# Performance work log

Measured on AMD Instinct MI355X. Metric: run time of the kernel, lower is better.

The kernel has to match this reference:

```python
import jax, jax.numpy as jnp
import numpy as np

S = 1024          # num tokens (single prefill sequence)
H = 2880          # hidden_size
NH = 64           # num query heads
NKV = 8           # num kv heads
HD = 64           # head_dim
G = NH // NKV     # query heads per kv head
THETA = 10000.0
SCALE = HD ** -0.5


def _rope(x, positions):
    # neox-style rotary over full head_dim; x: [S, n_heads, HD]
    half = HD // 2
    inv_freq = 1.0 / (THETA ** (jnp.arange(half, dtype=jnp.float32) / half))
    ang = positions.astype(jnp.float32)[:, None] * inv_freq          # [S, half]
    cos = jnp.cos(ang)[:, None, :]
    sin = jnp.sin(ang)[:, None, :]
    x1, x2 = x[..., :half], x[..., half:]
    return jnp.concatenate([x1 * cos - x2 * sin, x2 * cos + x1 * sin], axis=-1)


def setup_inputs() -> dict:
    key = jax.random.key(0)
    k0, k1, k2, k3 = jax.random.split(key, 4)
    return {
        "positions": jnp.arange(S, dtype=jnp.int32),
        "hidden_states": jax.random.normal(k0, (S, H), dtype=jnp.float32),
        "qkv_w": jax.random.normal(k1, ((NH + 2 * NKV) * HD, H), dtype=jnp.float32) * 0.02,
        "o_w": jax.random.normal(k2, (H, NH * HD), dtype=jnp.float32) * 0.02,
        "sinks": jax.random.normal(k3, (NH,), dtype=jnp.float32),
    }


def reference(positions, hidden_states, qkv_w, o_w, sinks):
    # fused QKV projection (no bias, matching attention_bias=False)
    qkv = hidden_states @ qkv_w.T                                     # [S, 5120]
    q = qkv[:, : NH * HD].reshape(S, NH, HD)
    k = qkv[:, NH * HD : NH * HD + NKV * HD].reshape(S, NKV, HD)
    v = qkv[:, NH * HD + NKV * HD :].reshape(S, NKV, HD)

    # rotary on q and k (rotary_dim == head_dim)
    q = _rope(q, positions)
    k = _rope(k, positions)

    # GQA: group query heads by kv head -> [S, NKV, G, HD]
    qg = q.reshape(S, NKV, G, HD)

    logits = jnp.einsum("qghd,kgd->ghqk", qg, k) * SCALE              # [NKV, G, S, S]
    causal = positions[:, None] >= positions[None, :]                 # [S, S]
    logits = jnp.where(causal[None, None], logits, -jnp.inf)

    # attention sinks: per-head extra logit in the softmax denominator,
    # contributing no value vector.
    sink = sinks.reshape(NKV, G)[:, :, None, None]                    # [NKV, G, 1, 1]
    m = jnp.maximum(jnp.max(logits, axis=-1, keepdims=True), sink)
    p = jnp.exp(logits - m)                                           # [NKV, G, S, S]
    denom = jnp.sum(p, axis=-1, keepdims=True) + jnp.exp(sink - m)
    attn = jnp.einsum("ghqk,kgd->qghd", p / denom, v)                 # [S, NKV, G, HD]

    out = attn.reshape(S, NH * HD) @ o_w.T                            # [S, H]
    return out
```

## Files before the change

### kernel.cpp

```cpp
#include <hip/hip_runtime.h>
#include <hip/hip_bf16.h>
#include <math.h>

#define S_LEN 1024
#define HDIM  2880
#define NH    64
#define NKV   8
#define HD    64
#define QKV_N ((NH + 2*NKV) * HD)
#define O_K   (NH * HD)
#define SCALE 0.125f

typedef _Float16 f16x8 __attribute__((ext_vector_type(8)));
typedef _Float16 f16x4 __attribute__((ext_vector_type(4)));
typedef float    f32x4 __attribute__((ext_vector_type(4)));

#define DMA16(GP, LP) __builtin_amdgcn_global_load_lds( \
        (const __attribute__((address_space(1))) void*)(GP), \
        (__attribute__((address_space(3))) void*)(LP), 16, 0, 0)

#define BARRIER() __builtin_amdgcn_s_barrier()
#define WAITV(n)  asm volatile("s_waitcnt vmcnt(" #n ")" ::: "memory")
#define WAITL()   asm volatile("s_waitcnt lgkmcnt(0)" ::: "memory")
#define SCHED0()  __builtin_amdgcn_sched_barrier(0)

__device__ __forceinline__ void cvt4(const float* __restrict__ s,
                                     _Float16* __restrict__ d, int i) {
    const float4 v = ((const float4*)s)[i];
    f16x4 p;
    p[0] = (_Float16)v.x; p[1] = (_Float16)v.y;
    p[2] = (_Float16)v.z; p[3] = (_Float16)v.w;
    ((f16x4*)d)[i] = p;
}

__global__ __launch_bounds__(256) void cvt_f32_f16(const float* __restrict__ src,
                                                   _Float16* __restrict__ dst, int n4) {
    const int stride = gridDim.x * blockDim.x;
    for (int i = blockIdx.x * blockDim.x + threadIdx.x; i < n4; i += stride)
        cvt4(src, dst, i);
}

__global__ __launch_bounds__(256) void cvt_all(const float* __restrict__ h,
                                               const float* __restrict__ qw,
                                               const float* __restrict__ ow,
                                               _Float16* __restrict__ dh,
                                               _Float16* __restrict__ dqw,
                                               _Float16* __restrict__ dow) {
    const int stride = gridDim.x * blockDim.x;
    const int t0 = blockIdx.x * blockDim.x + threadIdx.x;
    for (int i = t0; i < 737280;  i += stride) cvt4(h,  dh,  i);
    for (int i = t0; i < 3686400; i += stride) cvt4(qw, dqw, i);
    for (int i = t0; i < 2949120; i += stride) cvt4(ow, dow, i);
}

__device__ __forceinline__ f16x8 lds_frag(const _Float16* base, int row, int kf) {
    return *(const f16x8*)&base[row * 64 + (kf ^ ((row & 7) << 3))];
}

__device__ __forceinline__ void mfma_quad(f32x4 (&acc)[8][4], const f16x8 (&af)[4][2],
                                          const f16x8 (&bf)[2][2], int mh, int nh) {
    __builtin_amdgcn_s_setprio(1);
#pragma unroll
    for (int q4 = 0; q4 < 4; ++q4)
#pragma unroll
        for (int n2 = 0; n2 < 2; ++n2) {
            f32x4 a = acc[mh * 4 + q4][nh * 2 + n2];
            a = __builtin_amdgcn_mfma_f32_16x16x32_f16(af[q4][0], bf[n2][0], a, 0, 0, 0);
            a = __builtin_amdgcn_mfma_f32_16x16x32_f16(af[q4][1], bf[n2][1], a, 0, 0, 0);
            acc[mh * 4 + q4][nh * 2 + n2] = a;
        }
    __builtin_amdgcn_s_setprio(0);
}

__global__ __launch_bounds__(512, 2) void gemm_8p(const _Float16* __restrict__ A,
                                                  const _Float16* __restrict__ B,
                                                  _Float16* __restrict__ C,
                                                  int M, int N, int K) {
    __shared__ __align__(16) _Float16 sh[65536];

    const int tid  = threadIdx.x;
    const int lane = tid & 63;
    const int wave = tid >> 6;
    const int wr   = wave >> 2;
    const int wc   = wave & 3;
    const int quad = lane >> 4;
    const int fr   = lane & 15;
    const int row0 = blockIdx.y * 256;
    const int col0 = blockIdx.x * 256;

    const int klen = K / (int)gridDim.z;
    const int kb   = (int)blockIdx.z * klen;
    const int NT   = klen / 64;
    _Float16* Cp = C + (size_t)blockIdx.z * M * N;

    int    stDst[2];
    size_t aOff[2][2], bOff[2][2];
#pragma unroll
    for (int r = 0; r < 2; ++r) {
        const int c   = r * 512 + tid;
        const int row = c >> 3;
        const int sw  = ((c & 7) ^ (row & 7)) * 8;
        stDst[r] = (c & ~63) * 8;
#pragma unroll
        for (int h = 0; h < 2; ++h) {
            aOff[h][r] = (size_t)(row0 + h * 128 + row) * K + sw;
            int br = col0 + h * 128 + row; if (br > N - 1) br = N - 1;
            bOff[h][r] = (size_t)br * K + sw;
        }
    }
    const _Float16* Ab = A + kb;
    const _Float16* Bb = B + kb;

#define STAGE2(GB, OFF, LB) do { \
        DMA16((GB) + (OFF)[0], (LB) + stDst[0]); \
        DMA16((GB) + (OFF)[1], (LB) + stDst[1]); } while (0)

    f32x4 acc[8][4] = {};

    STAGE2(Ab, aOff[0], sh);
    STAGE2(Ab, aOff[1], sh + 8192);
    STAGE2(Bb, bOff[0], sh + 32768);
    STAGE2(Bb, bOff[1], sh + 32768 + 8192);
    if (NT > 1) {
        STAGE2(Ab + 64, aOff[0], sh + 16384);
        STAGE2(Ab + 64, aOff[1], sh + 16384 + 8192);
        WAITV(4);
    } else {
        WAITV(0);
    }
    BARRIER();

    for (int t = 0; t < NT; ++t) {
        _Float16* Ac = sh + ((t & 1) ? 16384 : 0);
        _Float16* Bc = sh + 32768 + ((t & 1) ? 16384 : 0);
        _Float16* Bn = sh + 32768 + ((t & 1) ? 0 : 16384);
        const bool st1 = (t + 1 < NT);
        const bool st2 = (t + 2 < NT);
        const int  k1  = (t + 1) * 64;
        const int  k2  = (t + 2) * 64;

        f16x8 aF0[4][2], aF1[4][2], bF[2][2];

#pragma unroll
        for (int q4 = 0; q4 < 4; ++q4) {
            const int row = wr * 128 + q4 * 16 + fr;
            aF0[q4][0] = lds_frag(Ac, row, quad * 8);
            aF0[q4][1] = lds_frag(Ac, row, 32 + quad * 8);
        }
#pragma unroll
        for (int n2 = 0; n2 < 2; ++n2) {
            const int row = wc * 64 + n2 * 16 + fr;
            bF[n2][0] = lds_frag(Bc, row, quad * 8);
            bF[n2][1] = lds_frag(Bc, row, 32 + quad * 8);
        }
        if (st1) STAGE2(Bb + k1, bOff[0], Bn);
        BARRIER(); WAITL(); SCHED0();
        mfma_quad(acc, aF0, bF, 0, 0);
        BARRIER();

#pragma unroll
        for (int q4 = 0; q4 < 4; ++q4) {
            const int row = wr * 128 + 64 + q4 * 16 + fr;
            aF1[q4][0] = lds_frag(Ac, row, quad * 8);
            aF1[q4][1] = lds_frag(Ac, row, 32 + quad * 8);
        }
        if (st1) STAGE2(Bb + k1, bOff[1], Bn + 8192);
        BARRIER(); WAITL(); SCHED0();
        mfma_quad(acc, aF1, bF, 1, 0);
        BARRIER();

#pragma unroll
        for (int n2 = 0; n2 < 2; ++n2) {
            const int row = wc * 64 + 32 + n2 * 16 + fr;
            bF[n2][0] = lds_frag(Bc, row, quad * 8);
            bF[n2][1] = lds_frag(Bc, row, 32 + quad * 8);
        }
        if (st2) STAGE2(Ab + k2, aOff[0], Ac);
        BARRIER(); WAITL(); SCHED0();
        mfma_quad(acc, aF1, bF, 1, 1);
        BARRIER();

        if (st2) {
            STAGE2(Ab + k2, aOff[1], Ac + 8192);
            WAITV(4);
        } else {
            WAITV(0);
        }
        BARRIER(); WAITL(); SCHED0();
        mfma_quad(acc, aF0, bF, 0, 1);
        BARRIER();
    }

    __syncthreads();
    _Float16* cbuf = sh;
#pragma unroll
    for (int h = 0; h < 2; ++h) {
        if (wr == h) {
#pragma unroll
            for (int mi = 0; mi < 8; ++mi)
#pragma unroll
                for (int ni = 0; ni < 4; ++ni) {
                    const f32x4 v = acc[mi][ni];
#pragma unroll
                    for (int rr = 0; rr < 4; ++rr)
                        cbuf[(mi * 16 + quad * 4 + rr) * 264 + wc * 64 + ni * 16 + fr] =
                            (_Float16)v[rr];
                }
        }
        __syncthreads();
#pragma unroll
        for (int u = 0; u < 8; ++u) {
            const int c    = u * 512 + tid;
            const int rowL = c >> 5;
            const int ch   = (c & 31) * 8;
            const int col  = col0 + ch;
            if (col < N)
                *(f16x8*)&Cp[(size_t)(row0 + h * 128 + rowL) * N + col] =
                    *(const f16x8*)&cbuf[rowL * 264 + ch];
        }
        __syncthreads();
    }
#undef STAGE2
}

#define CSTR 68
template<typename CT>
__global__ __launch_bounds__(256) void gemm_ff(const _Float16* __restrict__ A,
                                               const _Float16* __restrict__ B,
                                               CT* __restrict__ C,
                                               int M, int N, int K) {
    __shared__ __align__(16) _Float16 sh[16384];

    const int tid  = threadIdx.x;
    const int lane = tid & 63;
    const int wave = tid >> 6;
    const int wr   = wave >> 1;
    const int wc   = wave & 1;
    const int quad = lane >> 4;
    const int fr   = lane & 15;
    const int ks   = quad * 8;
    const int row0 = blockIdx.y * 128;
    const int col0 = blockIdx.x * 128;

    const int klen   = K / (int)gridDim.z;
    const int kb     = (int)blockIdx.z * klen;
    const int nsteps = klen / 32;
    CT* Cp = C + (size_t)blockIdx.z * M * N;

    const int r0   = tid >> 2;
    const int ch   = (tid & 3) * 8;
    const int dst0 = (tid & ~63) * 8;

    const size_t aoff0 = (size_t)(row0 + r0)      * K;
    const size_t aoff1 = (size_t)(row0 + r0 + 64) * K;
    int bR0 = col0 + r0;      if (bR0 >= N) bR0 = N - 1;
    int bR1 = col0 + r0 + 64; if (bR1 >= N) bR1 = N - 1;
    const size_t boff0 = (size_t)bR0 * K;
    const size_t boff1 = (size_t)bR1 * K;

    f32x4 acc[4][4] = {};

    {
        const int kk = kb + ch;
        DMA16(A + aoff0 + kk, sh + dst0);
        DMA16(A + aoff1 + kk, sh + 2048 + dst0);
        DMA16(B + boff0 + kk, sh + 8192 + dst0);
        DMA16(B + boff1 + kk, sh + 8192 + 2048 + dst0);
    }

    for (int step = 0; step < nsteps; ++step) {
        const int cur = step & 1;
        _Float16* Acur = sh + cur * 4096;
        _Float16* Anxt = sh + (cur ^ 1) * 4096;
        _Float16* Bcur = sh + 8192 + cur * 4096;
        _Float16* Bnxt = sh + 8192 + (cur ^ 1) * 4096;

        __syncthreads();

        if (step + 1 < nsteps) {
            const int k1 = kb + (step + 1) * 32 + ch;
            DMA16(A + aoff0 + k1, Anxt + dst0);
            DMA16(A + aoff1 + k1, Anxt + 2048 + dst0);
            DMA16(B + boff0 + k1, Bnxt + dst0);
            DMA16(B + boff1 + k1, Bnxt + 2048 + dst0);
        }

        f16x8 af[4], bf[4];
#pragma unroll
        for (int mi = 0; mi < 4; ++mi)
            af[mi] = *(const f16x8*)&Acur[(wr * 64 + mi * 16 + fr) * 32 + ks];
#pragma unroll
        for (int ni = 0; ni < 4; ++ni)
            bf[ni] = *(const f16x8*)&Bcur[(wc * 64 + ni * 16 + fr) * 32 + ks];
#pragma unroll
        for (int mi = 0; mi < 4; ++mi)
#pragma unroll
            for (int ni = 0; ni < 4; ++ni)
                acc[mi][ni] = __builtin_amdgcn_mfma_f32_16x16x32_f16(
                    af[mi], bf[ni], acc[mi][ni], 0, 0, 0);
    }

#pragma unroll
    for (int p = 0; p < 2; ++p) {
        __syncthreads();
        if (wc == p) {
#pragma unroll
            for (int mi = 0; mi < 4; ++mi)
#pragma unroll
                for (int ni = 0; ni < 4; ++ni) {
                    const f32x4 v = acc[mi][ni];
#pragma unroll
                    for (int r = 0; r < 4; ++r)
                        sh[(wr * 64 + mi * 16 + quad * 4 + r) * CSTR + ni * 16 + fr] =
                            (_Float16)v[r];
                }
        }
        __syncthreads();
#pragma unroll
        for (int it = 0; it < 4; ++it) {
            const int id  = it * 256 + tid;
            const int row = id >> 3;
            const int chh = (id & 7) * 8;
            const int col = col0 + p * 64 + chh;
            if (col < N) {
                const f16x4 lo = *(const f16x4*)&sh[row * CSTR + chh];
                const f16x4 hi = *(const f16x4*)&sh[row * CSTR + chh + 4];
                if constexpr (sizeof(CT) == 2) {
                    f16x8 v;
                    v[0]=lo[0]; v[1]=lo[1]; v[2]=lo[2]; v[3]=lo[3];
                    v[4]=hi[0]; v[5]=hi[1]; v[6]=hi[2]; v[7]=hi[3];
                    *(f16x8*)&Cp[(size_t)(row0 + row) * N + col] = v;
                } else {
                    float4 v0 = make_float4((float)lo[0], (float)lo[1],
                                            (float)lo[2], (float)lo[3]);
                    float4 v1 = make_float4((float)hi[0], (float)hi[1],
                                            (float)hi[2], (float)hi[3]);
                    *(float4*)&Cp[(size_t)(row0 + row) * N + col]     = v0;
                    *(float4*)&Cp[(size_t)(row0 + row) * N + col + 4] = v1;
                }
            }
        }
    }
}

template<typename CT>
__global__ __launch_bounds__(256) void gemm_f16(const _Float16* __restrict__ A,
                                                const float* __restrict__ B,
                                                CT* __restrict__ C,
                                                int M, int N, int K) {
    __shared__ __align__(16) _Float16 sh[16384];

    const int tid  = threadIdx.x;
    const int lane = tid & 63;
    const int wave = tid >> 6;
    const int wr   = wave >> 1;
    const int wc   = wave & 1;
    const int quad = lane >> 4;
    const int fr   = lane & 15;
    const int ks   = quad * 8;
    const int row0 = blockIdx.y * 128;
    const int col0 = blockIdx.x * 128;

    const int klen   = K / (int)gridDim.z;
    const int kb     = (int)blockIdx.z * klen;
    const int nsteps = klen / 32;
    CT* Cp = C + (size_t)blockIdx.z * M * N;

    const int a_cbase0 = wave * 64;
    const int a_ci0 = a_cbase0 + lane;
    const int a_r0 = a_ci0 >> 2, a_ch0 = a_ci0 & 3;
    const int a_cbase1 = 256 + wave * 64;
    const int a_ci1 = a_cbase1 + lane;
    const int a_r1 = a_ci1 >> 2, a_ch1 = a_ci1 & 3;
    int b_r[4], b_ch[4];
#pragma unroll
    for (int it = 0; it < 4; ++it) {
        const int c4 = it * 256 + tid;
        b_r[it]  = c4 >> 3;
        b_ch[it] = (c4 & 7) << 2;
    }

    float4 breg[4];
    f32x4 acc[4][4] = {};

    {
        const _Float16* gp0 = A + (size_t)(row0 + a_r0) * K + kb + a_ch0 * 8;
        DMA16(gp0, sh + (size_t)a_cbase0 * 8);
        const _Float16* gp1 = A + (size_t)(row0 + a_r1) * K + kb + a_ch1 * 8;
        DMA16(gp1, sh + (size_t)a_cbase1 * 8);
#pragma unroll
        for (int it = 0; it < 4; ++it) {
            int brow = col0 + b_r[it];
            if (brow >= N) brow = N - 1;
            breg[it] = *(const float4*)&B[(size_t)brow * K + kb + b_ch[it]];
        }
        _Float16* Bs0 = sh + 8192;
#pragma unroll
        for (int it = 0; it < 4; ++it) {
            f16x4 p;
            p[0] = (_Float16)breg[it].x; p[1] = (_Float16)breg[it].y;
            p[2] = (_Float16)breg[it].z; p[3] = (_Float16)breg[it].w;
            *(f16x4*)&Bs0[b_r[it] * 32 + b_ch[it]] = p;
        }
    }

    for (int step = 0; step < nsteps; ++step) {
        const int cur = step & 1;
        const int nxt = cur ^ 1;
        _Float16* Acur = sh + cur * 4096;
        _Float16* Anxt = sh + nxt * 4096;
        _Float16* Bcur = sh + 8192 + cur * 4096;
        _Float16* Bnxt = sh + 8192 + nxt * 4096;

        __syncthreads();

        const bool more = (step + 1 < nsteps);
        if (more) {
            const int k1 = kb + (step + 1) * 32;
            const _Float16* gp0 = A + (size_t)(row0 + a_r0) * K + k1 + a_ch0 * 8;
            DMA16(gp0, Anxt + (size_t)a_cbase0 * 8);
            const _Float16* gp1 = A + (size_t)(row0 + a_r1) * K + k1 + a_ch1 * 8;
            DMA16(gp1, Anxt + (size_t)a_cbase1 * 8);
#pragma unroll
            for (int it = 0; it < 4; ++it) {
                int brow = col0 + b_r[it];
                if (brow >= N) brow = N - 1;
                breg[it] = *(const float4*)&B[(size_t)brow * K + k1 + b_ch[it]];
            }
        }

        f16x8 af[4], bfr[4];
#pragma unroll
        for (int mi = 0; mi < 4; ++mi)
            af[mi] = *(const f16x8*)&Acur[(wr * 64 + mi * 16 + fr) * 32 + ks];
#pragma unroll
        for (int ni = 0; ni < 4; ++ni)
            bfr[ni] = *(const f16x8*)&Bcur[(wc * 64 + ni * 16 + fr) * 32 + ks];
#pragma unroll
        for (int mi = 0; mi < 4; ++mi)
#pragma unroll
            for (int ni = 0; ni < 4; ++ni)
                acc[mi][ni] = __builtin_amdgcn_mfma_f32_16x16x32_f16(
                    af[mi], bfr[ni], acc[mi][ni], 0, 0, 0);

        if (more) {
#pragma unroll
            for (int it = 0; it < 4; ++it) {
                f16x4 p;
                p[0] = (_Float16)breg[it].x; p[1] = (_Float16)breg[it].y;
                p[2] = (_Float16)breg[it].z; p[3] = (_Float16)breg[it].w;
                *(f16x4*)&Bnxt[b_r[it] * 32 + b_ch[it]] = p;
            }
        }
    }

#pragma unroll
    for (int p = 0; p < 2; ++p) {
        __syncthreads();
        if (wc == p) {
#pragma unroll
            for (int mi = 0; mi < 4; ++mi)
#pragma unroll
                for (int ni = 0; ni < 4; ++ni) {
                    const f32x4 v = acc[mi][ni];
#pragma unroll
                    for (int r = 0; r < 4; ++r)
                        sh[(wr * 64 + mi * 16 + quad * 4 + r) * CSTR + ni * 16 + fr] =
                            (_Float16)v[r];
                }
        }
        __syncthreads();
#pragma unroll
        for (int it = 0; it < 4; ++it) {
            const int id  = it * 256 + tid;
            const int row = id >> 3;
            const int chh = (id & 7) * 8;
            const int col = col0 + p * 64 + chh;
            if (col < N) {
                const f16x4 lo = *(const f16x4*)&sh[row * CSTR + chh];
                const f16x4 hi = *(const f16x4*)&sh[row * CSTR + chh + 4];
                if constexpr (sizeof(CT) == 2) {
                    f16x8 v;
                    v[0]=lo[0]; v[1]=lo[1]; v[2]=lo[2]; v[3]=lo[3];
                    v[4]=hi[0]; v[5]=hi[1]; v[6]=hi[2]; v[7]=hi[3];
                    *(f16x8*)&Cp[(size_t)(row0 + row) * N + col] = v;
                } else {
                    float4 v0 = make_float4((float)lo[0], (float)lo[1],
                                            (float)lo[2], (float)lo[3]);
                    float4 v1 = make_float4((float)hi[0], (float)hi[1],
                                            (float)hi[2], (float)hi[3]);
                    *(float4*)&Cp[(size_t)(row0 + row) * N + col]     = v0;
                    *(float4*)&Cp[(size_t)(row0 + row) * N + col + 4] = v1;
                }
            }
        }
    }
}

__global__ __launch_bounds__(256) void rope_reduce(_Float16* __restrict__ parts,
                                                   int nsplit,
                                                   _Float16* __restrict__ vt,
                                                   const int* __restrict__ positions) {
    __shared__ float buf[QKV_N];
    const int s   = blockIdx.x;
    const int tid = threadIdx.x;
    const size_t PSTR = (size_t)S_LEN * QKV_N;

    for (int c = tid; c < QKV_N / 4; c += 256) {
        float4 a = make_float4(0.f, 0.f, 0.f, 0.f);
        for (int j = 0; j < nsplit; ++j) {
            const f16x4 v = ((const f16x4*)(parts + j * PSTR + (size_t)s * QKV_N))[c];
            a.x += (float)v[0]; a.y += (float)v[1];
            a.z += (float)v[2]; a.w += (float)v[3];
        }
        ((float4*)buf)[c] = a;
    }
    __syncthreads();

    const float pos = (float)positions[s];
    _Float16* orow = parts + (size_t)s * QKV_N;
    for (int w = tid; w < 72 * 32; w += 256) {
        const int h = w >> 5;
        const int t = w & 31;
        const float inv_freq = exp2f(-(float)t * (13.287712379549449f / 32.0f));
        const float ang = pos * inv_freq;
        float sn, cs;
        sincosf(ang, &sn, &cs);
        const float x1 = buf[h * 64 + t];
        const float x2 = buf[h * 64 + t + 32];
        orow[h * 64 + t]      = (_Float16)(x1 * cs - x2 * sn);
        orow[h * 64 + t + 32] = (_Float16)(x2 * cs + x1 * sn);
    }
    for (int c = tid; c < NKV * HD; c += 256)
        vt[(size_t)c * S_LEN + s] = (_Float16)buf[(NH + NKV) * HD + c];
}

__global__ __launch_bounds__(256) void o_reduce(const _Float16* __restrict__ parts,
                                                float* __restrict__ out,
                                                int n4, int nsplit) {
    const size_t PSTR = (size_t)S_LEN * HDIM;
    const int stride = gridDim.x * blockDim.x;
    for (int i = blockIdx.x * blockDim.x + threadIdx.x; i < n4; i += stride) {
        float4 a = make_float4(0.f, 0.f, 0.f, 0.f);
        for (int j = 0; j < nsplit; ++j) {
            const f16x4 v = ((const f16x4*)(parts + j * PSTR))[i];
            a.x += (float)v[0]; a.y += (float)v[1];
            a.z += (float)v[2]; a.w += (float)v[3];
        }
        ((float4*)out)[i] = a;
    }
}

#define LSTR 72
__global__ __launch_bounds__(256) void attn_mfma(const _Float16* __restrict__ qkv,
                                                 const _Float16* __restrict__ vt,
                                                 const float* __restrict__ sinks,
                                                 const int* __restrict__ positions,
                                                 _Float16* __restrict__ attn_out) {
    __shared__ __align__(16) _Float16 Ks[2][64 * LSTR];
    __shared__ __align__(16) _Float16 Vs[2][64 * LSTR];
    __shared__ __align__(16) _Float16 Ps[64 * LSTR];

    const int tid  = threadIdx.x;
    const int lane = tid & 63;
    const int wave = tid >> 6;
    const int fr   = lane & 15;
    const int quad = lane >> 4;
    const int ks8  = quad * 8;
    const int n    = blockIdx.x;
    const int qt   = (int)gridDim.y - 1 - (int)blockIdx.y;
    const int g    = n >> 3;

    int st_r[2], st_o[2];
#pragma unroll
    for (int it = 0; it < 2; ++it) {
        const int c = it * 256 + tid;
        st_r[it] = c >> 3;
        st_o[it] = (c & 7) * 8;
    }

    const _Float16* qrow = qkv + (size_t)(qt * 64 + wave * 16 + fr) * QKV_N + n * HD;
    const f16x8 a_q0 = *(const f16x8*)&qrow[ks8];
    const f16x8 a_q1 = *(const f16x8*)&qrow[32 + ks8];

    int pq[4];
#pragma unroll
    for (int r = 0; r < 4; ++r)
        pq[r] = positions[qt * 64 + wave * 16 + quad * 4 + r];

    const float sinkv = sinks[n];
    float m[4], l[4];
    f32x4 o[4] = {};
#pragma unroll
    for (int r = 0; r < 4; ++r) { m[r] = sinkv; l[r] = 1.0f; }

    f16x8 kreg[2], vreg[2];
    {
        const _Float16* Kg = qkv + (size_t)0 * QKV_N + NH * HD + g * HD;
        const _Float16* Vg = vt + (size_t)(g * HD) * S_LEN;
#pragma unroll
        for (int it = 0; it < 2; ++it) {
            kreg[it] = *(const f16x8*)&Kg[(size_t)st_r[it] * QKV_N + st_o[it]];
            vreg[it] = *(const f16x8*)&Vg[(size_t)st_r[it] * S_LEN + st_o[it]];
        }
#pragma unroll
        for (int it = 0; it < 2; ++it) {
            *(f16x8*)&Ks[0][st_r[it] * LSTR + st_o[it]] = kreg[it];
            *(f16x8*)&Vs[0][st_r[it] * LSTR + st_o[it]] = vreg[it];
        }
    }

    for (int kt = 0; kt <= qt; ++kt) {
        const int cur = kt & 1;
        const int nxt = cur ^ 1;
        __syncthreads();

        const bool more = (kt < qt);
        if (more) {
            const _Float16* Kg = qkv + (size_t)((kt + 1) * 64) * QKV_N + NH * HD + g * HD;
            const _Float16* Vg = vt + (size_t)(g * HD) * S_LEN + (kt + 1) * 64;
#pragma unroll
            for (int it = 0; it < 2; ++it) {
                kreg[it] = *(const f16x8*)&Kg[(size_t)st_r[it] * QKV_N + st_o[it]];
                vreg[it] = *(const f16x8*)&Vg[(size_t)st_r[it] * S_LEN + st_o[it]];
            }
        }

        f32x4 s[4] = {};
#pragma unroll
        for (int nt = 0; nt < 4; ++nt) {
            const f16x8 b0 = *(const f16x8*)&Ks[cur][(nt * 16 + fr) * LSTR + ks8];
            s[nt] = __builtin_amdgcn_mfma_f32_16x16x32_f16(a_q0, b0, s[nt], 0, 0, 0);
            const f16x8 b1 = *(const f16x8*)&Ks[cur][(nt * 16 + fr) * LSTR + 32 + ks8];
            s[nt] = __builtin_amdgcn_mfma_f32_16x16x32_f16(a_q1, b1, s[nt], 0, 0, 0);
        }

        const bool diag = (kt == qt);
        int pk[4];
        if (diag) {
#pragma unroll
            for (int nt = 0; nt < 4; ++nt) pk[nt] = positions[qt * 64 + nt * 16 + fr];
        }
#pragma unroll
        for (int nt = 0; nt < 4; ++nt)
#pragma unroll
            for (int r = 0; r < 4; ++r) {
                float sv = s[nt][r] * SCALE;
                if (diag && pk[nt] > pq[r]) sv = -3.0e38f;
                s[nt][r] = sv;
            }

#pragma unroll
        for (int r = 0; r < 4; ++r) {
            float tm = fmaxf(fmaxf(s[0][r], s[1][r]), fmaxf(s[2][r], s[3][r]));
            tm = fmaxf(tm, __shfl_xor(tm, 1, 64));
            tm = fmaxf(tm, __shfl_xor(tm, 2, 64));
            tm = fmaxf(tm, __shfl_xor(tm, 4, 64));
            tm = fmaxf(tm, __shfl_xor(tm, 8, 64));
            const float nm = fmaxf(m[r], tm);
            const float alpha = __expf(m[r] - nm);
            float rs = 0.0f;
#pragma unroll
            for (int nt = 0; nt < 4; ++nt) {
                const float p = __expf(s[nt][r] - nm);
                s[nt][r] = p;
                rs += p;
            }
            rs += __shfl_xor(rs, 1, 64);
            rs += __shfl_xor(rs, 2, 64);
            rs += __shfl_xor(rs, 4, 64);
            rs += __shfl_xor(rs, 8, 64);
            l[r] = l[r] * alpha + rs;
            m[r] = nm;
#pragma unroll
            for (int nt = 0; nt < 4; ++nt) o[nt][r] *= alpha;
        }

#pragma unroll
        for (int nt = 0; nt < 4; ++nt)
#pragma unroll
            for (int r = 0; r < 4; ++r)
                Ps[(wave * 16 + quad * 4 + r) * LSTR + nt * 16 + fr] = (_Float16)s[nt][r];
        __threadfence_block();

#pragma unroll
        for (int k2 = 0; k2 < 2; ++k2) {
            const f16x8 ap = *(const f16x8*)&Ps[(wave * 16 + fr) * LSTR + k2 * 32 + ks8];
#pragma unroll
            for (int nt = 0; nt < 4; ++nt) {
                const f16x8 bv = *(const f16x8*)&Vs[cur][(nt * 16 + fr) * LSTR + k2 * 32 + ks8];
                o[nt] = __builtin_amdgcn_mfma_f32_16x16x32_f16(ap, bv, o[nt], 0, 0, 0);
            }
        }

        if (more) {
#pragma unroll
            for (int it = 0; it < 2; ++it) {
                *(f16x8*)&Ks[nxt][st_r[it] * LSTR + st_o[it]] = kreg[it];
                *(f16x8*)&Vs[nxt][st_r[it] * LSTR + st_o[it]] = vreg[it];
            }
        }
    }

#pragma unroll
    for (int r = 0; r < 4; ++r) {
        const float inv = 1.0f / l[r];
        const size_t row = (size_t)(qt * 64 + wave * 16 + quad * 4 + r);
#pragma unroll
        for (int nt = 0; nt < 4; ++nt)
            attn_out[row * O_K + n * HD + nt * 16 + fr] = (_Float16)(o[nt][r] * inv);
    }
}

extern "C" void kernel_launch(void* const* d_in, const int* in_sizes, int n_in,
                              void* d_out, int out_size, void* d_ws, size_t ws_size,
                              hipStream_t stream) {
    const int*   positions = (const int*)d_in[0];
    const float* hidden    = (const float*)d_in[1];
    const float* qkv_w     = (const float*)d_in[2];
    const float* o_w       = (const float*)d_in[3];
    const float* sinks     = (const float*)d_in[4];
    float* out = (float*)d_out;

    const size_t n_hid  = (size_t)S_LEN * HDIM;
    const size_t n_qkv  = (size_t)S_LEN * QKV_N;
    const size_t n_attn = (size_t)S_LEN * O_K;
    const size_t n_vt   = (size_t)NKV * HD * S_LEN;
    const size_t n_out  = (size_t)S_LEN * HDIM;
    const size_t n_qw   = (size_t)QKV_N * HDIM;
    const size_t n_ow   = (size_t)HDIM * O_K;

    const int SP_Q = 3;
    const int SP_O = 4;

    const size_t need_full =
        (n_hid + SP_Q * n_qkv + n_attn + n_vt + n_qw + n_ow) * sizeof(_Float16);
    const size_t need_mid  = (n_hid + SP_Q * n_qkv + n_attn + n_vt) * sizeof(_Float16);

    if (ws_size >= need_full) {
        _Float16* hid_h  = (_Float16*)d_ws;
        _Float16* qkvp   = hid_h + n_hid;
        _Float16* attn_h = qkvp + SP_Q * n_qkv;
        _Float16* vt     = attn_h + n_attn;
        _Float16* qw_h   = vt + n_vt;
        _Float16* ow_h   = qw_h + n_qw;
        _Float16* opart  = qkvp;

        cvt_all<<<2048, 256, 0, stream>>>(hidden, qkv_w, o_w, hid_h, qw_h, ow_h);
        gemm_8p<<<dim3(QKV_N / 256, S_LEN / 256, SP_Q), 512, 0, stream>>>(
            hid_h, qw_h, qkvp, S_LEN, QKV_N, HDIM);
        rope_reduce<<<S_LEN, 256, 0, stream>>>(qkvp, SP_Q, vt, positions);
        attn_mfma<<<dim3(NH, S_LEN / 64), 256, 0, stream>>>(qkvp, vt, sinks, positions, attn_h);
        gemm_8p<<<dim3((HDIM + 255) / 256, S_LEN / 256, SP_O), 512, 0, stream>>>(
            attn_h, ow_h, opart, S_LEN, HDIM, O_K);
        o_reduce<<<1024, 256, 0, stream>>>(opart, out, (int)(n_out / 4), SP_O);
    } else if (ws_size >= need_mid) {
        _Float16* hid_h  = (_Float16*)d_ws;
        _Float16* qkvp   = hid_h + n_hid;
        _Float16* attn_h = qkvp + SP_Q * n_qkv;
        _Float16* vt     = attn_h + n_attn;
        _Float16* opart  = qkvp;

        cvt_f32_f16<<<512, 256, 0, stream>>>(hidden, hid_h, (int)(n_hid / 4));
        gemm_f16<_Float16><<<dim3(QKV_N / 128, S_LEN / 128, SP_Q), 256, 0, stream>>>(
            hid_h, qkv_w, qkvp, S_LEN, QKV_N, HDIM);
        rope_reduce<<<S_LEN, 256, 0, stream>>>(qkvp, SP_Q, vt, positions);
        attn_mfma<<<dim3(NH, S_LEN / 64), 256, 0, stream>>>(qkvp, vt, sinks, positions, attn_h);
        gemm_f16<_Float16><<<dim3((HDIM + 127) / 128, S_LEN / 128, SP_O), 256, 0, stream>>>(
            attn_h, o_w, opart, S_LEN, HDIM, O_K);
        o_reduce<<<1024, 256, 0, stream>>>(opart, out, (int)(n_out / 4), SP_O);
    } else {
        _Float16* hid_h  = (_Float16*)d_ws;
        _Float16* qkvp   = hid_h + n_hid;
        _Float16* attn_h = qkvp + n_qkv;
        _Float16* vt     = attn_h + n_attn;

        cvt_f32_f16<<<512, 256, 0, stream>>>(hidden, hid_h, (int)(n_hid / 4));
        gemm_f16<_Float16><<<dim3(QKV_N / 128, S_LEN / 128, 1), 256, 0, stream>>>(
            hid_h, qkv_w, qkvp, S_LEN, QKV_N, HDIM);
        rope_reduce<<<S_LEN, 256, 0, stream>>>(qkvp, 1, vt, positions);
        attn_mfma<<<dim3(NH, S_LEN / 64), 256, 0, stream>>>(qkvp, vt, sinks, positions, attn_h);
        gemm_f16<float><<<dim3((HDIM + 127) / 128, S_LEN / 128, 1), 256, 0, stream>>>(
            attn_h, o_w, out, S_LEN, HDIM, O_K);
    }
}
```

Measured before the change: 268.5 us.

## Move o_w fp16 conversion into attention kernel and unroll conversion loops

The fp32-to-fp16 conversion of the output-projection weight moves out of the upfront conversion kernel and into the start of the attention kernel. There, every attention block converts a strided slice before doing its own work, so this memory-bound copy can overlap with the compute-bound attention. The conversion loops are also unrolled four-way so each thread has more loads in flight. The cost is extra register pressure and a longer prologue in the attention kernel, which could slow its main loop or its occupancy.

```diff
diff --git a/kernel.cpp b/kernel.cpp
--- a/kernel.cpp
+++ b/kernel.cpp
@@ -24,33 +24,48 @@
 #define WAITL()   asm volatile("s_waitcnt lgkmcnt(0)" ::: "memory")
 #define SCHED0()  __builtin_amdgcn_sched_barrier(0)
 
-__device__ __forceinline__ void cvt4(const float* __restrict__ s,
-                                     _Float16* __restrict__ d, int i) {
-    const float4 v = ((const float4*)s)[i];
+__device__ __forceinline__ void cvt_st4(_Float16* __restrict__ d, int i,
+                                        const float4 v) {
     f16x4 p;
     p[0] = (_Float16)v.x; p[1] = (_Float16)v.y;
     p[2] = (_Float16)v.z; p[3] = (_Float16)v.w;
     ((f16x4*)d)[i] = p;
 }
 
+__device__ __forceinline__ void cvt_range(const float* __restrict__ s,
+                                          _Float16* __restrict__ d,
+                                          int n4, int t0, int stride) {
+    int i = t0;
+    for (; i + 3 * stride < n4; i += 4 * stride) {
+        const float4 v0 = ((const float4*)s)[i];
+        const float4 v1 = ((const float4*)s)[i + stride];
+        const float4 v2 = ((const float4*)s)[i + 2 * stride];
+        const float4 v3 = ((const float4*)s)[i + 3 * stride];
+        cvt_st4(d, i,              v0);
+        cvt_st4(d, i + stride,     v1);
+        cvt_st4(d, i + 2 * stride, v2);
+        cvt_st4(d, i + 3 * stride, v3);
+    }
+    for (; i < n4; i += stride) {
+        const float4 v = ((const float4*)s)[i];
+        cvt_st4(d, i, v);
+    }
+}
+
 __global__ __launch_bounds__(256) void cvt_f32_f16(const float* __restrict__ src,
                                                    _Float16* __restrict__ dst, int n4) {
-    const int stride = gridDim.x * blockDim.x;
-    for (int i = blockIdx.x * blockDim.x + threadIdx.x; i < n4; i += stride)
-        cvt4(src, dst, i);
-}
-
-__global__ __launch_bounds__(256) void cvt_all(const float* __restrict__ h,
-                                               const float* __restrict__ qw,
-                                               const float* __restrict__ ow,
-                                               _Float16* __restrict__ dh,
-                                               _Float16* __restrict__ dqw,
-                                               _Float16* __restrict__ dow) {
+    cvt_range(src, dst, n4, blockIdx.x * blockDim.x + threadIdx.x,
+              gridDim.x * blockDim.x);
+}
+
+__global__ __launch_bounds__(256) void cvt_hq(const float* __restrict__ h,
+                                              const float* __restrict__ qw,
+                                              _Float16* __restrict__ dh,
+                                              _Float16* __restrict__ dqw) {
     const int stride = gridDim.x * blockDim.x;
     const int t0 = blockIdx.x * blockDim.x + threadIdx.x;
-    for (int i = t0; i < 737280;  i += stride) cvt4(h,  dh,  i);
-    for (int i = t0; i < 3686400; i += stride) cvt4(qw, dqw, i);
-    for (int i = t0; i < 2949120; i += stride) cvt4(ow, dow, i);
+    cvt_range(h,  dh,  737280,  t0, stride);
+    cvt_range(qw, dqw, 3686400, t0, stride);
 }
 
 __device__ __forceinline__ f16x8 lds_frag(const _Float16* base, int row, int kf) {
@@ -556,7 +571,9 @@
                                                  const _Float16* __restrict__ vt,
                                                  const float* __restrict__ sinks,
                                                  const int* __restrict__ positions,
-                                                 _Float16* __restrict__ attn_out) {
+                                                 _Float16* __restrict__ attn_out,
+                                                 const float* __restrict__ ow_src,
+                                                 _Float16* __restrict__ ow_dst) {
     __shared__ __align__(16) _Float16 Ks[2][64 * LSTR];
     __shared__ __align__(16) _Float16 Vs[2][64 * LSTR];
     __shared__ __align__(16) _Float16 Ps[64 * LSTR];
@@ -570,6 +587,12 @@
     const int n    = blockIdx.x;
     const int qt   = (int)gridDim.y - 1 - (int)blockIdx.y;
     const int g    = n >> 3;
+
+    if (ow_src) {
+        const int nthr = (int)(gridDim.x * gridDim.y) * 256;
+        const int t0   = ((int)blockIdx.y * (int)gridDim.x + (int)blockIdx.x) * 256 + tid;
+        cvt_range(ow_src, ow_dst, HDIM * O_K / 4, t0, nthr);
+    }
 
     int st_r[2], st_o[2];
 #pragma unroll
@@ -746,11 +769,12 @@
         _Float16* ow_h   = qw_h + n_qw;
         _Float16* opart  = qkvp;
 
-        cvt_all<<<2048, 256, 0, stream>>>(hidden, qkv_w, o_w, hid_h, qw_h, ow_h);
+        cvt_hq<<<1024, 256, 0, stream>>>(hidden, qkv_w, hid_h, qw_h);
         gemm_8p<<<dim3(QKV_N / 256, S_LEN / 256, SP_Q), 512, 0, stream>>>(
             hid_h, qw_h, qkvp, S_LEN, QKV_N, HDIM);
         rope_reduce<<<S_LEN, 256, 0, stream>>>(qkvp, SP_Q, vt, positions);
-        attn_mfma<<<dim3(NH, S_LEN / 64), 256, 0, stream>>>(qkvp, vt, sinks, positions, attn_h);
+        attn_mfma<<<dim3(NH, S_LEN / 64), 256, 0, stream>>>(
+            qkvp, vt, sinks, positions, attn_h, o_w, ow_h);
         gemm_8p<<<dim3((HDIM + 255) / 256, S_LEN / 256, SP_O), 512, 0, stream>>>(
             attn_h, ow_h, opart, S_LEN, HDIM, O_K);
         o_reduce<<<1024, 256, 0, stream>>>(opart, out, (int)(n_out / 4), SP_O);
@@ -765,7 +789,8 @@
         gemm_f16<_Float16><<<dim3(QKV_N / 128, S_LEN / 128, SP_Q), 256, 0, stream>>>(
             hid_h, qkv_w, qkvp, S_LEN, QKV_N, HDIM);
         rope_reduce<<<S_LEN, 256, 0, stream>>>(qkvp, SP_Q, vt, positions);
-        attn_mfma<<<dim3(NH, S_LEN / 64), 256, 0, stream>>>(qkvp, vt, sinks, positions, attn_h);
+        attn_mfma<<<dim3(NH, S_LEN / 64), 256, 0, stream>>>(
+            qkvp, vt, sinks, positions, attn_h, nullptr, nullptr);
         gemm_f16<_Float16><<<dim3((HDIM + 127) / 128, S_LEN / 128, SP_O), 256, 0, stream>>>(
             attn_h, o_w, opart, S_LEN, HDIM, O_K);
         o_reduce<<<1024, 256, 0, stream>>>(opart, out, (int)(n_out / 4), SP_O);
@@ -779,7 +804,8 @@
         gemm_f16<_Float16><<<dim3(QKV_N / 128, S_LEN / 128, 1), 256, 0, stream>>>(
             hid_h, qkv_w, qkvp, S_LEN, QKV_N, HDIM);
         rope_reduce<<<S_LEN, 256, 0, stream>>>(qkvp, 1, vt, positions);
-        attn_mfma<<<dim3(NH, S_LEN / 64), 256, 0, stream>>>(qkvp, vt, sinks, positions, attn_h);
+        attn_mfma<<<dim3(NH, S_LEN / 64), 256, 0, stream>>>(
+            qkvp, vt, sinks, positions, attn_h, nullptr, nullptr);
         gemm_f16<float><<<dim3((HDIM + 127) / 128, S_LEN / 128, 1), 256, 0, stream>>>(
             attn_h, o_w, out, S_LEN, HDIM, O_K);
     }
```

Result: no change. 272.7 us (+1.5%).
